# Kernel optimization log

Measured on AMD Instinct MI355X. Metric: run time of the kernel, lower is better.

The kernel has to match this reference:

```python
import jax, jax.numpy as jnp
import numpy as np

N = 20000          # nodes
E = 320000         # edges
G = 256            # g_dim
H1 = 256           # h1_dim (RGCN out)
H2 = 128           # h2_dim (per-head transformer out)
HEADS = 4
R = 8              # num relations
EPS_BN = 1e-5


def setup_inputs() -> dict:
    key = jax.random.key(0)
    ks = jax.random.split(key, 16)
    inp = {
        "node_features": jax.random.normal(ks[0], (N, G), jnp.float32),
        "node_type": jax.random.randint(ks[1], (N,), 0, 3),
        "edge_index": jax.random.randint(ks[2], (2, E), 0, N),
        "edge_type": jax.random.randint(ks[3], (E,), 0, R),
        # RGCNConv params
        "W_rel": jax.random.normal(ks[4], (R, G, H1), jnp.float32) * (1.0 / np.sqrt(G)),
        "W_root": jax.random.normal(ks[5], (G, H1), jnp.float32) * (1.0 / np.sqrt(G)),
        "b_rgcn": jnp.zeros((H1,), jnp.float32),
        # TransformerConv params (concat=True -> HEADS*H2 output)
        "W_q": jax.random.normal(ks[6], (H1, HEADS * H2), jnp.float32) * (1.0 / np.sqrt(H1)),
        "b_q": jnp.zeros((HEADS * H2,), jnp.float32),
        "W_k": jax.random.normal(ks[7], (H1, HEADS * H2), jnp.float32) * (1.0 / np.sqrt(H1)),
        "b_k": jnp.zeros((HEADS * H2,), jnp.float32),
        "W_v": jax.random.normal(ks[8], (H1, HEADS * H2), jnp.float32) * (1.0 / np.sqrt(H1)),
        "b_v": jnp.zeros((HEADS * H2,), jnp.float32),
        "W_skip": jax.random.normal(ks[9], (H1, HEADS * H2), jnp.float32) * (1.0 / np.sqrt(H1)),
        "b_skip": jnp.zeros((HEADS * H2,), jnp.float32),
        # BatchNorm1d params (training-mode batch stats)
        "bn_gamma": jnp.ones((HEADS * H2,), jnp.float32),
        "bn_beta": jnp.zeros((HEADS * H2,), jnp.float32),
    }
    return inp


def reference(node_features, node_type, edge_index, edge_type,
              W_rel, W_root, b_rgcn,
              W_q, b_q, W_k, b_k, W_v, b_v, W_skip, b_skip,
              bn_gamma, bn_beta):
    x = node_features
    src, dst = edge_index[0], edge_index[1]  # messages flow src -> dst

    # ---- RGCNConv (mean aggregation per relation, root weight, bias) ----
    xr = jnp.einsum('nd,rdh->nrh', x, W_rel)           # (N, R, H1)
    msg = xr[src, edge_type]                            # (E, H1)
    seg = dst * R + edge_type                           # combined (node, relation) segment id
    sums = jax.ops.segment_sum(msg, seg, num_segments=N * R)
    cnt = jax.ops.segment_sum(jnp.ones((E,), x.dtype), seg, num_segments=N * R)
    mean = sums / jnp.maximum(cnt, 1.0)[:, None]
    agg = mean.reshape(N, R, H1).sum(axis=1)            # sum over relations
    h1 = agg + x @ W_root + b_rgcn                      # (N, H1)

    # ---- TransformerConv (heads=HEADS, concat=True, root skip) ----
    q = (h1 @ W_q + b_q).reshape(N, HEADS, H2)
    k = (h1 @ W_k + b_k).reshape(N, HEADS, H2)
    v = (h1 @ W_v + b_v).reshape(N, HEADS, H2)

    scale = 1.0 / np.sqrt(H2)
    alpha = jnp.sum(q[dst] * k[src], axis=-1) * scale   # (E, HEADS)
    amax = jax.ops.segment_max(alpha, dst, num_segments=N)  # per-dst softmax max
    ea = jnp.exp(alpha - amax[dst])
    denom = jax.ops.segment_sum(ea, dst, num_segments=N)
    attn = ea / jnp.maximum(denom[dst], 1e-16)          # (E, HEADS)

    out = jax.ops.segment_sum(attn[:, :, None] * v[src], dst, num_segments=N)
    out = out.reshape(N, HEADS * H2) + h1 @ W_skip + b_skip

    # ---- BatchNorm1d (batch stats) + LeakyReLU(0.01) ----
    mu = out.mean(axis=0)
    var = out.var(axis=0)
    xn = (out - mu) * jax.lax.rsqrt(var + EPS_BN)
    y = bn_gamma * xn + bn_beta
    return jax.nn.leaky_relu(y, negative_slope=0.01)
```

## Files before the change

### kernel.cpp

```cpp
#include <hip/hip_runtime.h>

static const int N_NODES = 20000;
static const int N_EDGES = 320000;
static const int GDIM    = 256;
static const int H1DIM   = 256;
static const int C2DIM   = 512;
static const int NREL    = 8;
static const int NSEG    = N_NODES * NREL;

typedef _Float16 __attribute__((ext_vector_type(8))) half8;
typedef _Float16 __attribute__((ext_vector_type(4))) half4;
typedef __attribute__((ext_vector_type(4))) float f32x4;

__device__ __forceinline__ void gload_lds16(const void* g, void* l) {
  __builtin_amdgcn_global_load_lds(
      (const __attribute__((address_space(1))) unsigned int*)g,
      (__attribute__((address_space(3))) unsigned int*)l, 16, 0, 0);
}

__device__ __forceinline__ void swz_bxy(int& bx, int& by) {
  int nx   = gridDim.x;
  int nwg  = nx * gridDim.y;
  int orig = blockIdx.y * nx + blockIdx.x;
  int xcd  = orig & 7;
  int q    = nwg >> 3, r = nwg & 7;
  int base = xcd < r ? xcd * (q + 1) : r * (q + 1) + (xcd - r) * q;
  int wgid = base + (orig >> 3);
  bx = wgid % nx; by = wgid / nx;
}


template<int OUT_HALF>
__global__ __launch_bounds__(256) void gemm_mfma_k(
    const _Float16* __restrict__ A, const _Float16* __restrict__ Bt,
    const float* __restrict__ bias, void* __restrict__ Cout,
    int M, int N, int K)
{
  __shared__ _Float16 As[128 * 64];
  __shared__ _Float16 Bs[128 * 64];
  int bx, by; swz_bxy(bx, by);
  const int tid  = threadIdx.x;
  const int wid  = tid >> 6, lane = tid & 63;
  const int wr   = wid >> 1, wc = wid & 1;
  const int brow = by * 128;
  const int bcol = bx * 128;
  const int l15  = lane & 15, lhi = lane >> 4;
  const int srow = wid * 32;
  const int lrow = lane >> 3;
  const int lchk = lane & 7;

  f32x4 acc[4][4] = {};

  for (int k0 = 0; k0 < K; k0 += 64) {
    __syncthreads();
#pragma unroll
    for (int i = 0; i < 4; ++i) {
      int row = srow + i * 8 + lrow;
      int gc  = lchk ^ (row & 7);
      gload_lds16(A  + (size_t)(brow + row) * K + k0 + gc * 8,
                  &As[(srow + i * 8) * 64]);
      gload_lds16(Bt + (size_t)(bcol + row) * K + k0 + gc * 8,
                  &Bs[(srow + i * 8) * 64]);
    }
    __syncthreads();
#pragma unroll
    for (int kf = 0; kf < 2; ++kf) {
      int cc = kf * 4 + lhi;
      half8 af[4], bfr[4];
#pragma unroll
      for (int mi = 0; mi < 4; ++mi) {
        int row = wr * 64 + mi * 16 + l15;
        af[mi] = ((const half8*)As)[row * 8 + (cc ^ (row & 7))];
      }
#pragma unroll
      for (int ni = 0; ni < 4; ++ni) {
        int row = wc * 64 + ni * 16 + l15;
        bfr[ni] = ((const half8*)Bs)[row * 8 + (cc ^ (row & 7))];
      }
#pragma unroll
      for (int mi = 0; mi < 4; ++mi)
#pragma unroll
        for (int ni = 0; ni < 4; ++ni)
          acc[mi][ni] = __builtin_amdgcn_mfma_f32_16x16x32_f16(
              af[mi], bfr[ni], acc[mi][ni], 0, 0, 0);
    }
  }
#pragma unroll
  for (int ni = 0; ni < 4; ++ni) {
    int col = bcol + wc * 64 + ni * 16 + l15;
    float bb = bias ? bias[col] : 0.f;
#pragma unroll
    for (int mi = 0; mi < 4; ++mi) {
      int row0 = brow + wr * 64 + mi * 16 + lhi * 4;
#pragma unroll
      for (int j = 0; j < 4; ++j) {
        int r = row0 + j;
        if (r >= M) continue;
        float val = acc[mi][ni][j] + bb;
        if (OUT_HALF) ((_Float16*)Cout)[(size_t)r * N + col] = (_Float16)val;
        else          ((float*)Cout)[(size_t)r * N + col] = val;
      }
    }
  }
}

__global__ __launch_bounds__(256) void gemm_qkvs_k(
    const _Float16* __restrict__ A, const _Float16* __restrict__ Bt,
    const float* __restrict__ bias_cat,
    float* __restrict__ qbuf, _Float16* __restrict__ kbuf,
    _Float16* __restrict__ vbuf, float* __restrict__ outp, int M)
{
  const int K = 256, N = 2048;
  __shared__ _Float16 As[128 * 64];
  __shared__ _Float16 Bs[128 * 64];
  int bx, by; swz_bxy(bx, by);
  const int tid  = threadIdx.x;
  const int wid  = tid >> 6, lane = tid & 63;
  const int wr   = wid >> 1, wc = wid & 1;
  const int brow = by * 128;
  const int bcol = bx * 128;
  const int l15  = lane & 15, lhi = lane >> 4;
  const int srow = wid * 32;
  const int lrow = lane >> 3;
  const int lchk = lane & 7;

  f32x4 acc[4][4] = {};

  for (int k0 = 0; k0 < K; k0 += 64) {
    __syncthreads();
#pragma unroll
    for (int i = 0; i < 4; ++i) {
      int row = srow + i * 8 + lrow;
      int gc  = lchk ^ (row & 7);
      gload_lds16(A  + (size_t)(brow + row) * K + k0 + gc * 8,
                  &As[(srow + i * 8) * 64]);
      gload_lds16(Bt + (size_t)(bcol + row) * K + k0 + gc * 8,
                  &Bs[(srow + i * 8) * 64]);
    }
    __syncthreads();
#pragma unroll
    for (int kf = 0; kf < 2; ++kf) {
      int cc = kf * 4 + lhi;
      half8 af[4], bfr[4];
#pragma unroll
      for (int mi = 0; mi < 4; ++mi) {
        int row = wr * 64 + mi * 16 + l15;
        af[mi] = ((const half8*)As)[row * 8 + (cc ^ (row & 7))];
      }
#pragma unroll
      for (int ni = 0; ni < 4; ++ni) {
        int row = wc * 64 + ni * 16 + l15;
        bfr[ni] = ((const half8*)Bs)[row * 8 + (cc ^ (row & 7))];
      }
#pragma unroll
      for (int mi = 0; mi < 4; ++mi)
#pragma unroll
        for (int ni = 0; ni < 4; ++ni)
          acc[mi][ni] = __builtin_amdgcn_mfma_f32_16x16x32_f16(
              af[mi], bfr[ni], acc[mi][ni], 0, 0, 0);
    }
  }
#pragma unroll
  for (int ni = 0; ni < 4; ++ni) {
    int colbase = bcol + wc * 64 + ni * 16;
    int sel = colbase >> 9;
    int c   = (colbase & 511) + l15;
    float bb = bias_cat[colbase + l15];
#pragma unroll
    for (int mi = 0; mi < 4; ++mi) {
      int row0 = brow + wr * 64 + mi * 16 + lhi * 4;
#pragma unroll
      for (int j = 0; j < 4; ++j) {
        int r = row0 + j;
        if (r >= M) continue;
        float val = acc[mi][ni][j] + bb;
        if      (sel == 0) qbuf[(size_t)r * 512 + c] = val;
        else if (sel == 1) kbuf[(size_t)r * 512 + c] = (_Float16)val;
        else if (sel == 2) vbuf[(size_t)r * 512 + c] = (_Float16)val;
        else               outp[(size_t)r * 512 + c] = val;
      }
    }
  }
}

__global__ void conv_wcat_k(const float* __restrict__ W_root, const float* __restrict__ W_rel,
                            _Float16* __restrict__ Wt)
{
  int k = blockIdx.x * 256 + threadIdx.x;
  int n = blockIdx.y;
  float v = (k < 256) ? W_root[(size_t)k * H1DIM + n]
                      : W_rel[(size_t)(k - 256) * H1DIM + n];
  Wt[(size_t)n * 2304 + k] = (_Float16)v;
}

__global__ void conv_wqkvs_k(const float* __restrict__ Wq, const float* __restrict__ Wk,
                             const float* __restrict__ Wv, const float* __restrict__ Ws,
                             const float* __restrict__ bq, const float* __restrict__ bk,
                             const float* __restrict__ bv, const float* __restrict__ bs,
                             _Float16* __restrict__ Wt, float* __restrict__ bias_cat)
{
  int k = threadIdx.x;
  int n = blockIdx.y;
  int sel = n >> 9, c = n & 511;
  const float* W = sel == 0 ? Wq : sel == 1 ? Wk : sel == 2 ? Wv : Ws;
  Wt[(size_t)n * 256 + k] = (_Float16)W[(size_t)k * C2DIM + c];
  if (k == 0) {
    const float* B = sel == 0 ? bq : sel == 1 ? bk : sel == 2 ? bv : bs;
    bias_cat[n] = B[c];
  }
}

__global__ void conv_xh_k(const float* __restrict__ x, _Float16* __restrict__ xh)
{
  int i = blockIdx.x * blockDim.x + threadIdx.x;
  if (i >= N_NODES * GDIM / 4) return;
  float4 v = ((const float4*)x)[i];
  half4 o = {(_Float16)v.x, (_Float16)v.y, (_Float16)v.z, (_Float16)v.w};
  ((half4*)xh)[i] = o;
}

__global__ void hist_k(const int* __restrict__ dst, const int* __restrict__ et,
                       int* __restrict__ h)
{
  int e = blockIdx.x * blockDim.x + threadIdx.x;
  if (e >= N_EDGES) return;
  atomicAdd(&h[dst[e] * NREL + et[e]], 1);
}

__global__ __launch_bounds__(1024) void scan_local_k(
    const int* __restrict__ in, int* __restrict__ out, int* __restrict__ bsum, int n)
{
  __shared__ int s[1024];
  int gi = blockIdx.x * 1024 + threadIdx.x;
  int v = gi < n ? in[gi] : 0;
  s[threadIdx.x] = v; __syncthreads();
  for (int off = 1; off < 1024; off <<= 1) {
    int t = threadIdx.x >= off ? s[threadIdx.x - off] : 0;
    __syncthreads();
    s[threadIdx.x] += t;
    __syncthreads();
  }
  if (gi < n) out[gi] = s[threadIdx.x] - v;
  if (threadIdx.x == 1023) bsum[blockIdx.x] = s[1023];
}

__global__ __launch_bounds__(1024) void scan_small_k(int* __restrict__ bsum, int nb)
{
  __shared__ int s[1024];
  int v = threadIdx.x < nb ? bsum[threadIdx.x] : 0;
  s[threadIdx.x] = v; __syncthreads();
  for (int off = 1; off < 1024; off <<= 1) {
    int t = threadIdx.x >= off ? s[threadIdx.x - off] : 0;
    __syncthreads();
    s[threadIdx.x] += t;
    __syncthreads();
  }
  if (threadIdx.x < nb) bsum[threadIdx.x] = s[threadIdx.x] - v;
}

__global__ void scan_addoff_k(int* __restrict__ out, const int* __restrict__ bsum, int n)
{
  int gi = blockIdx.x * 1024 + threadIdx.x;
  if (gi < n) out[gi] += bsum[blockIdx.x];
}

__global__ void initcur_k(int* __restrict__ off, int* __restrict__ cur)
{
  int i = blockIdx.x * blockDim.x + threadIdx.x;
  if (i < NSEG) cur[i] = off[i];
  if (i == 0) off[NSEG] = N_EDGES;
}

__global__ void reorder_k(const int* __restrict__ src, const int* __restrict__ dst,
                          const int* __restrict__ et,
                          int* __restrict__ cur, int* __restrict__ esrc)
{
  int e = blockIdx.x * blockDim.x + threadIdx.x;
  if (e >= N_EDGES) return;
  int s = src[e];
  int seg = dst[e] * NREL + et[e];
  esrc[atomicAdd(&cur[seg], 1)] = s;
}

__global__ __launch_bounds__(256) void agg_xcat_k(
    const _Float16* __restrict__ xh, const int* __restrict__ off,
    const int* __restrict__ esrc, _Float16* __restrict__ Xcat)
{
  int d = blockIdx.x * 4 + (threadIdx.x >> 6);
  if (d >= N_NODES) return;
  int lane = threadIdx.x & 63;
  _Float16* xrow = Xcat + (size_t)d * 2304;
  half4 xv = ((const half4*)(xh + (size_t)d * GDIM))[lane];
  *(half4*)(xrow + lane * 4) = xv;
  for (int r = 0; r < NREL; ++r) {
    int seg = d * NREL + r;
    int beg = off[seg], end = off[seg + 1];
    float4 acc = make_float4(0.f, 0.f, 0.f, 0.f);
    for (int e = beg; e < end; ++e) {
      int s = esrc[e];
      half4 v = ((const half4*)(xh + (size_t)s * GDIM))[lane];
      acc.x += (float)v.x; acc.y += (float)v.y;
      acc.z += (float)v.z; acc.w += (float)v.w;
    }
    float inv = (end > beg) ? 1.0f / (float)(end - beg) : 0.0f;
    half4 o;
    o.x = (_Float16)(acc.x * inv); o.y = (_Float16)(acc.y * inv);
    o.z = (_Float16)(acc.z * inv); o.w = (_Float16)(acc.w * inv);
    *(half4*)(xrow + 256 + r * 256 + lane * 4) = o;
  }
}

__global__ __launch_bounds__(256) void attn_fused_k(
    const float* __restrict__ q, const _Float16* __restrict__ kb,
    const _Float16* __restrict__ vb,
    const int* __restrict__ off, const int* __restrict__ esrc,
    float* __restrict__ out)
{
  int d = blockIdx.x * 4 + (threadIdx.x >> 6);
  if (d >= N_NODES) return;
  int lane = threadIdx.x & 63;
  const float4* qrow = (const float4*)(q + (size_t)d * C2DIM);
  float4 q0 = qrow[lane * 2], q1 = qrow[lane * 2 + 1];
  float qf[8] = {q0.x, q0.y, q0.z, q0.w, q1.x, q1.y, q1.z, q1.w};
  float m = -3.4e38f, ssum = 0.f;
  float av[8] = {};
  int beg = off[d * NREL], end = off[d * NREL + NREL];
  half8 krN = {}, vrN = {};
  if (beg < end) {
    int s0 = esrc[beg];
    krN = ((const half8*)(kb + (size_t)s0 * C2DIM))[lane];
    vrN = ((const half8*)(vb + (size_t)s0 * C2DIM))[lane];
  }
  for (int e = beg; e < end; ++e) {
    half8 kr = krN, vr = vrN;
    if (e + 1 < end) {
      int s1 = esrc[e + 1];
      krN = ((const half8*)(kb + (size_t)s1 * C2DIM))[lane];
      vrN = ((const half8*)(vb + (size_t)s1 * C2DIM))[lane];
    }
    float p = 0.f;
#pragma unroll
    for (int j = 0; j < 8; ++j) p += qf[j] * (float)kr[j];
    p += __shfl_xor(p, 1); p += __shfl_xor(p, 2);
    p += __shfl_xor(p, 4); p += __shfl_xor(p, 8);
    float a = p * 0.08838834764831845f;
    float mn = fmaxf(m, a);
    float corr = __expf(m - mn), w = __expf(a - mn);
    ssum = ssum * corr + w;
#pragma unroll
    for (int j = 0; j < 8; ++j) av[j] = av[j] * corr + w * (float)vr[j];
    m = mn;
  }
  float inv = 1.0f / fmaxf(ssum, 1e-16f);
  float* orow = out + (size_t)d * C2DIM + lane * 8;
#pragma unroll
  for (int j = 0; j < 8; ++j) orow[j] += av[j] * inv;
}

__global__ __launch_bounds__(512) void bn_stats_k(
    const float* __restrict__ x, float* __restrict__ sums, float* __restrict__ sumsq)
{
  int c = threadIdx.x;
  float s = 0.f, sq = 0.f;
  for (int row = blockIdx.x; row < N_NODES; row += gridDim.x) {
    float v = x[(size_t)row * C2DIM + c];
    s += v; sq += v * v;
  }
  atomicAdd(&sums[c], s);
  atomicAdd(&sumsq[c], sq);
}

__global__ void bn_final_k(const float* __restrict__ sums, const float* __restrict__ sumsq,
                           const float* __restrict__ gamma, const float* __restrict__ beta,
                           float* __restrict__ scale, float* __restrict__ shift)
{
  int c = threadIdx.x;
  float mu  = sums[c] * (1.0f / N_NODES);
  float var = sumsq[c] * (1.0f / N_NODES) - mu * mu;
  float sc  = gamma[c] * rsqrtf(var + 1e-5f);
  scale[c] = sc;
  shift[c] = beta[c] - mu * sc;
}

__global__ void bn_apply_k(float* __restrict__ x, const float* __restrict__ scale,
                           const float* __restrict__ shift, int total)
{
  int i = blockIdx.x * blockDim.x + threadIdx.x;
  if (i >= total) return;
  int c = i & (C2DIM - 1);
  float v = x[i] * scale[c] + shift[c];
  x[i] = v >= 0.f ? v : 0.01f * v;
}

extern "C" void kernel_launch(void* const* d_in, const int* in_sizes, int n_in,
                              void* d_out, int out_size, void* d_ws, size_t ws_size,
                              hipStream_t stream)
{
  const float* x      = (const float*)d_in[0];
  const int*   ei     = (const int*)d_in[2];
  const int*   src    = ei;
  const int*   dst    = ei + N_EDGES;
  const int*   etype  = (const int*)d_in[3];
  const float* W_rel  = (const float*)d_in[4];
  const float* W_root = (const float*)d_in[5];
  const float* b_rgcn = (const float*)d_in[6];
  const float* W_q = (const float*)d_in[7];  const float* b_q = (const float*)d_in[8];
  const float* W_k = (const float*)d_in[9];  const float* b_k = (const float*)d_in[10];
  const float* W_v = (const float*)d_in[11]; const float* b_v = (const float*)d_in[12];
  const float* W_s = (const float*)d_in[13]; const float* b_s = (const float*)d_in[14];
  const float* gamma = (const float*)d_in[15];
  const float* beta  = (const float*)d_in[16];
  float* out = (float*)d_out;

  char* ws = (char*)d_ws;
  _Float16* Xcat   = (_Float16*)(ws + 0);
  float*    qbuf   = (float*)(ws + 0);
  _Float16* kbuf   = (_Float16*)(ws + 40960000);
  _Float16* vbuf   = (_Float16*)(ws + 61440000);
  _Float16* Wt_cat = (_Float16*)(ws + 92160000);
  _Float16* Wt_qk  = (_Float16*)(ws + 93339648);
  _Float16* h1h    = (_Float16*)(ws + 94388224);
  _Float16* xh     = h1h;

  char* C = ws + 104628224;
  int*   cur      = (int*)(C + 0);
  int*   off      = (int*)(C + 640000);
  int*   esrc     = (int*)(C + 1280016);
  int*   bsum     = (int*)(C + 2560016);
  float* bns      = (float*)(C + 2564112);
  float* bias_cat = (float*)(C + 2572304);
  float* bnsum = bns, *bnsq = bns + 512, *bnscale = bns + 1024, *bnshift = bns + 1536;

  hipMemsetAsync(C, 0, 640000, stream);
  hipMemsetAsync(bns, 0, 8192, stream);

  dim3 blk(256);
  const int NB = (NSEG + 1023) / 1024;

  hist_k<<<dim3((N_EDGES + 255) / 256), blk, 0, stream>>>(dst, etype, cur);
  scan_local_k<<<dim3(NB), dim3(1024), 0, stream>>>(cur, off, bsum, NSEG);
  scan_small_k<<<dim3(1), dim3(1024), 0, stream>>>(bsum, NB);
  scan_addoff_k<<<dim3(NB), dim3(1024), 0, stream>>>(off, bsum, NSEG);
  initcur_k<<<dim3((NSEG + 255) / 256), blk, 0, stream>>>(off, cur);
  reorder_k<<<dim3((N_EDGES + 255) / 256), blk, 0, stream>>>(
      src, dst, etype, cur, esrc);

  conv_wcat_k<<<dim3(9, 256), blk, 0, stream>>>(W_root, W_rel, Wt_cat);
  conv_wqkvs_k<<<dim3(1, 2048), blk, 0, stream>>>(
      W_q, W_k, W_v, W_s, b_q, b_k, b_v, b_s, Wt_qk, bias_cat);
  conv_xh_k<<<dim3((N_NODES * GDIM / 4 + 255) / 256), blk, 0, stream>>>(x, xh);

  agg_xcat_k<<<dim3((N_NODES + 3) / 4), blk, 0, stream>>>(xh, off, esrc, Xcat);

  gemm_mfma_k<1><<<dim3(H1DIM / 128, (N_NODES + 127) / 128), blk, 0, stream>>>(
      Xcat, Wt_cat, b_rgcn, h1h, N_NODES, H1DIM, 2304);

  gemm_qkvs_k<<<dim3(2048 / 128, (N_NODES + 127) / 128), blk, 0, stream>>>(
      h1h, Wt_qk, bias_cat, qbuf, kbuf, vbuf, out, N_NODES);

  attn_fused_k<<<dim3((N_NODES + 3) / 4), blk, 0, stream>>>(
      qbuf, kbuf, vbuf, off, esrc, out);

  bn_stats_k<<<dim3(208), dim3(512), 0, stream>>>(out, bnsum, bnsq);
  bn_final_k<<<dim3(1), dim3(512), 0, stream>>>(bnsum, bnsq, gamma, beta, bnscale, bnshift);
  bn_apply_k<<<dim3((N_NODES * C2DIM + 255) / 256), blk, 0, stream>>>(
      out, bnscale, bnshift, N_NODES * C2DIM);
}
```

Measured before the change: 391.4 us.

## Merge prep kernels, store QKVS interleaved in fp16, fuse BN finalize and skip add

Merges the histogram, the weight transposes and the x-to-half conversion into one prep kernel, and folds initcur into scan_addoff. The QKVS GEMM now writes one interleaved fp16 row per node through the generic GEMM. Attention reads q, k, v and skip from that buffer and writes the output directly instead of read-modify-write. BatchNorm finalize moves into a vectorized apply kernel. Together these remove several launches and a memset and cut memory traffic, at the cost of fp16 precision for q and the skip path.

```diff
diff --git a/kernel.cpp b/kernel.cpp
--- a/kernel.cpp
+++ b/kernel.cpp
@@ -28,7 +28,6 @@
   int wgid = base + (orig >> 3);
   bx = wgid % nx; by = wgid / nx;
 }
-
 
 template<int OUT_HALF>
 __global__ __launch_bounds__(256) void gemm_mfma_k(
@@ -104,127 +103,43 @@
   }
 }
 
-__global__ __launch_bounds__(256) void gemm_qkvs_k(
-    const _Float16* __restrict__ A, const _Float16* __restrict__ Bt,
-    const float* __restrict__ bias_cat,
-    float* __restrict__ qbuf, _Float16* __restrict__ kbuf,
-    _Float16* __restrict__ vbuf, float* __restrict__ outp, int M)
-{
-  const int K = 256, N = 2048;
-  __shared__ _Float16 As[128 * 64];
-  __shared__ _Float16 Bs[128 * 64];
-  int bx, by; swz_bxy(bx, by);
-  const int tid  = threadIdx.x;
-  const int wid  = tid >> 6, lane = tid & 63;
-  const int wr   = wid >> 1, wc = wid & 1;
-  const int brow = by * 128;
-  const int bcol = bx * 128;
-  const int l15  = lane & 15, lhi = lane >> 4;
-  const int srow = wid * 32;
-  const int lrow = lane >> 3;
-  const int lchk = lane & 7;
-
-  f32x4 acc[4][4] = {};
-
-  for (int k0 = 0; k0 < K; k0 += 64) {
-    __syncthreads();
-#pragma unroll
-    for (int i = 0; i < 4; ++i) {
-      int row = srow + i * 8 + lrow;
-      int gc  = lchk ^ (row & 7);
-      gload_lds16(A  + (size_t)(brow + row) * K + k0 + gc * 8,
-                  &As[(srow + i * 8) * 64]);
-      gload_lds16(Bt + (size_t)(bcol + row) * K + k0 + gc * 8,
-                  &Bs[(srow + i * 8) * 64]);
-    }
-    __syncthreads();
-#pragma unroll
-    for (int kf = 0; kf < 2; ++kf) {
-      int cc = kf * 4 + lhi;
-      half8 af[4], bfr[4];
-#pragma unroll
-      for (int mi = 0; mi < 4; ++mi) {
-        int row = wr * 64 + mi * 16 + l15;
-        af[mi] = ((const half8*)As)[row * 8 + (cc ^ (row & 7))];
-      }
-#pragma unroll
-      for (int ni = 0; ni < 4; ++ni) {
-        int row = wc * 64 + ni * 16 + l15;
-        bfr[ni] = ((const half8*)Bs)[row * 8 + (cc ^ (row & 7))];
-      }
-#pragma unroll
-      for (int mi = 0; mi < 4; ++mi)
-#pragma unroll
-        for (int ni = 0; ni < 4; ++ni)
-          acc[mi][ni] = __builtin_amdgcn_mfma_f32_16x16x32_f16(
-              af[mi], bfr[ni], acc[mi][ni], 0, 0, 0);
-    }
-  }
-#pragma unroll
-  for (int ni = 0; ni < 4; ++ni) {
-    int colbase = bcol + wc * 64 + ni * 16;
-    int sel = colbase >> 9;
-    int c   = (colbase & 511) + l15;
-    float bb = bias_cat[colbase + l15];
-#pragma unroll
-    for (int mi = 0; mi < 4; ++mi) {
-      int row0 = brow + wr * 64 + mi * 16 + lhi * 4;
-#pragma unroll
-      for (int j = 0; j < 4; ++j) {
-        int r = row0 + j;
-        if (r >= M) continue;
-        float val = acc[mi][ni][j] + bb;
-        if      (sel == 0) qbuf[(size_t)r * 512 + c] = val;
-        else if (sel == 1) kbuf[(size_t)r * 512 + c] = (_Float16)val;
-        else if (sel == 2) vbuf[(size_t)r * 512 + c] = (_Float16)val;
-        else               outp[(size_t)r * 512 + c] = val;
-      }
-    }
-  }
-}
-
-__global__ void conv_wcat_k(const float* __restrict__ W_root, const float* __restrict__ W_rel,
-                            _Float16* __restrict__ Wt)
-{
-  int k = blockIdx.x * 256 + threadIdx.x;
-  int n = blockIdx.y;
-  float v = (k < 256) ? W_root[(size_t)k * H1DIM + n]
-                      : W_rel[(size_t)(k - 256) * H1DIM + n];
-  Wt[(size_t)n * 2304 + k] = (_Float16)v;
-}
-
-__global__ void conv_wqkvs_k(const float* __restrict__ Wq, const float* __restrict__ Wk,
-                             const float* __restrict__ Wv, const float* __restrict__ Ws,
-                             const float* __restrict__ bq, const float* __restrict__ bk,
-                             const float* __restrict__ bv, const float* __restrict__ bs,
-                             _Float16* __restrict__ Wt, float* __restrict__ bias_cat)
-{
-  int k = threadIdx.x;
-  int n = blockIdx.y;
-  int sel = n >> 9, c = n & 511;
-  const float* W = sel == 0 ? Wq : sel == 1 ? Wk : sel == 2 ? Wv : Ws;
-  Wt[(size_t)n * 256 + k] = (_Float16)W[(size_t)k * C2DIM + c];
-  if (k == 0) {
-    const float* B = sel == 0 ? bq : sel == 1 ? bk : sel == 2 ? bv : bs;
-    bias_cat[n] = B[c];
-  }
-}
-
-__global__ void conv_xh_k(const float* __restrict__ x, _Float16* __restrict__ xh)
-{
-  int i = blockIdx.x * blockDim.x + threadIdx.x;
-  if (i >= N_NODES * GDIM / 4) return;
-  float4 v = ((const float4*)x)[i];
-  half4 o = {(_Float16)v.x, (_Float16)v.y, (_Float16)v.z, (_Float16)v.w};
-  ((half4*)xh)[i] = o;
-}
-
-__global__ void hist_k(const int* __restrict__ dst, const int* __restrict__ et,
-                       int* __restrict__ h)
-{
-  int e = blockIdx.x * blockDim.x + threadIdx.x;
-  if (e >= N_EDGES) return;
-  atomicAdd(&h[dst[e] * NREL + et[e]], 1);
+__global__ __launch_bounds__(256) void prep_k(
+    const int* __restrict__ dst, const int* __restrict__ et, int* __restrict__ hist,
+    const float* __restrict__ W_root, const float* __restrict__ W_rel,
+    _Float16* __restrict__ Wt_cat,
+    const float* __restrict__ Wq, const float* __restrict__ Wk,
+    const float* __restrict__ Wv, const float* __restrict__ Ws,
+    const float* __restrict__ bq, const float* __restrict__ bk,
+    const float* __restrict__ bv, const float* __restrict__ bs,
+    _Float16* __restrict__ Wt_qk, float* __restrict__ bias_cat,
+    const float* __restrict__ x, _Float16* __restrict__ xh)
+{
+  int b = blockIdx.x, tid = threadIdx.x;
+  if (b < 1250) {
+    int e = b * 256 + tid;
+    if (e < N_EDGES) atomicAdd(&hist[dst[e] * NREL + et[e]], 1);
+  } else if (b < 3554) {
+    int idx = (b - 1250) * 256 + tid;
+    int k = idx % 2304, n = idx / 2304;
+    float v = (k < 256) ? W_root[(size_t)k * H1DIM + n]
+                        : W_rel[(size_t)(k - 256) * H1DIM + n];
+    Wt_cat[(size_t)n * 2304 + k] = (_Float16)v;
+  } else if (b < 5602) {
+    int idx = (b - 3554) * 256 + tid;
+    int n = idx >> 8, k = idx & 255;
+    int sel = n >> 9, c = n & 511;
+    const float* W = sel == 0 ? Wq : sel == 1 ? Wk : sel == 2 ? Wv : Ws;
+    Wt_qk[(size_t)n * 256 + k] = (_Float16)W[(size_t)k * C2DIM + c];
+    if (k == 0) {
+      const float* B = sel == 0 ? bq : sel == 1 ? bk : sel == 2 ? bv : bs;
+      bias_cat[n] = B[c];
+    }
+  } else {
+    int i = (b - 5602) * 256 + tid;
+    float4 v = ((const float4*)x)[i];
+    half4 o = {(_Float16)v.x, (_Float16)v.y, (_Float16)v.z, (_Float16)v.w};
+    ((half4*)xh)[i] = o;
+  }
 }
 
 __global__ __launch_bounds__(1024) void scan_local_k(
@@ -258,17 +173,16 @@
   if (threadIdx.x < nb) bsum[threadIdx.x] = s[threadIdx.x] - v;
 }
 
-__global__ void scan_addoff_k(int* __restrict__ out, const int* __restrict__ bsum, int n)
+__global__ void scan_addoff_k(int* __restrict__ off, const int* __restrict__ bsum,
+                              int* __restrict__ cur, int n)
 {
   int gi = blockIdx.x * 1024 + threadIdx.x;
-  if (gi < n) out[gi] += bsum[blockIdx.x];
-}
-
-__global__ void initcur_k(int* __restrict__ off, int* __restrict__ cur)
-{
-  int i = blockIdx.x * blockDim.x + threadIdx.x;
-  if (i < NSEG) cur[i] = off[i];
-  if (i == 0) off[NSEG] = N_EDGES;
+  if (gi < n) {
+    int v = off[gi] + bsum[blockIdx.x];
+    off[gi] = v;
+    cur[gi] = v;
+  }
+  if (gi == 0) off[n] = N_EDGES;
 }
 
 __global__ void reorder_k(const int* __restrict__ src, const int* __restrict__ dst,
@@ -277,9 +191,8 @@
 {
   int e = blockIdx.x * blockDim.x + threadIdx.x;
   if (e >= N_EDGES) return;
-  int s = src[e];
   int seg = dst[e] * NREL + et[e];
-  esrc[atomicAdd(&cur[seg], 1)] = s;
+  esrc[atomicAdd(&cur[seg], 1)] = src[e];
 }
 
 __global__ __launch_bounds__(256) void agg_xcat_k(
@@ -311,32 +224,34 @@
 }
 
 __global__ __launch_bounds__(256) void attn_fused_k(
-    const float* __restrict__ q, const _Float16* __restrict__ kb,
-    const _Float16* __restrict__ vb,
+    const _Float16* __restrict__ qkvs,
     const int* __restrict__ off, const int* __restrict__ esrc,
     float* __restrict__ out)
 {
   int d = blockIdx.x * 4 + (threadIdx.x >> 6);
   if (d >= N_NODES) return;
   int lane = threadIdx.x & 63;
-  const float4* qrow = (const float4*)(q + (size_t)d * C2DIM);
-  float4 q0 = qrow[lane * 2], q1 = qrow[lane * 2 + 1];
-  float qf[8] = {q0.x, q0.y, q0.z, q0.w, q1.x, q1.y, q1.z, q1.w};
+  half8 qr = ((const half8*)(qkvs + (size_t)d * 2048))[lane];
+  float qf[8];
+#pragma unroll
+  for (int j = 0; j < 8; ++j) qf[j] = (float)qr[j];
   float m = -3.4e38f, ssum = 0.f;
   float av[8] = {};
   int beg = off[d * NREL], end = off[d * NREL + NREL];
   half8 krN = {}, vrN = {};
   if (beg < end) {
     int s0 = esrc[beg];
-    krN = ((const half8*)(kb + (size_t)s0 * C2DIM))[lane];
-    vrN = ((const half8*)(vb + (size_t)s0 * C2DIM))[lane];
+    const half8* row = (const half8*)(qkvs + (size_t)s0 * 2048 + 512);
+    krN = row[lane];
+    vrN = row[64 + lane];
   }
   for (int e = beg; e < end; ++e) {
     half8 kr = krN, vr = vrN;
     if (e + 1 < end) {
       int s1 = esrc[e + 1];
-      krN = ((const half8*)(kb + (size_t)s1 * C2DIM))[lane];
-      vrN = ((const half8*)(vb + (size_t)s1 * C2DIM))[lane];
+      const half8* row = (const half8*)(qkvs + (size_t)s1 * 2048 + 512);
+      krN = row[lane];
+      vrN = row[64 + lane];
     }
     float p = 0.f;
 #pragma unroll
@@ -352,9 +267,10 @@
     m = mn;
   }
   float inv = 1.0f / fmaxf(ssum, 1e-16f);
+  half8 sr = ((const half8*)(qkvs + (size_t)d * 2048 + 1536))[lane];
   float* orow = out + (size_t)d * C2DIM + lane * 8;
 #pragma unroll
-  for (int j = 0; j < 8; ++j) orow[j] += av[j] * inv;
+  for (int j = 0; j < 8; ++j) orow[j] = av[j] * inv + (float)sr[j];
 }
 
 __global__ __launch_bounds__(512) void bn_stats_k(
@@ -370,26 +286,26 @@
   atomicAdd(&sumsq[c], sq);
 }
 
-__global__ void bn_final_k(const float* __restrict__ sums, const float* __restrict__ sumsq,
+__global__ void bn_apply_k(float* __restrict__ x,
+                           const float* __restrict__ sums, const float* __restrict__ sumsq,
                            const float* __restrict__ gamma, const float* __restrict__ beta,
-                           float* __restrict__ scale, float* __restrict__ shift)
-{
-  int c = threadIdx.x;
-  float mu  = sums[c] * (1.0f / N_NODES);
-  float var = sumsq[c] * (1.0f / N_NODES) - mu * mu;
-  float sc  = gamma[c] * rsqrtf(var + 1e-5f);
-  scale[c] = sc;
-  shift[c] = beta[c] - mu * sc;
-}
-
-__global__ void bn_apply_k(float* __restrict__ x, const float* __restrict__ scale,
-                           const float* __restrict__ shift, int total)
+                           int total4)
 {
   int i = blockIdx.x * blockDim.x + threadIdx.x;
-  if (i >= total) return;
-  int c = i & (C2DIM - 1);
-  float v = x[i] * scale[c] + shift[c];
-  x[i] = v >= 0.f ? v : 0.01f * v;
+  if (i >= total4) return;
+  int c0 = (i & 127) * 4;
+  float4 v = ((const float4*)x)[i];
+  float o[4] = {v.x, v.y, v.z, v.w};
+#pragma unroll
+  for (int j = 0; j < 4; ++j) {
+    int c = c0 + j;
+    float mu  = sums[c] * (1.0f / N_NODES);
+    float var = sumsq[c] * (1.0f / N_NODES) - mu * mu;
+    float sc  = gamma[c] * rsqrtf(var + 1e-5f);
+    float val = (o[j] - mu) * sc + beta[c];
+    o[j] = val >= 0.f ? val : 0.01f * val;
+  }
+  ((float4*)x)[i] = make_float4(o[0], o[1], o[2], o[3]);
 }
 
 extern "C" void kernel_launch(void* const* d_in, const int* in_sizes, int n_in,
@@ -414,9 +330,7 @@
 
   char* ws = (char*)d_ws;
   _Float16* Xcat   = (_Float16*)(ws + 0);
-  float*    qbuf   = (float*)(ws + 0);
-  _Float16* kbuf   = (_Float16*)(ws + 40960000);
-  _Float16* vbuf   = (_Float16*)(ws + 61440000);
+  _Float16* QKVS   = (_Float16*)(ws + 0);
   _Float16* Wt_cat = (_Float16*)(ws + 92160000);
   _Float16* Wt_qk  = (_Float16*)(ws + 93339648);
   _Float16* h1h    = (_Float16*)(ws + 94388224);
@@ -424,45 +338,41 @@
 
   char* C = ws + 104628224;
   int*   cur      = (int*)(C + 0);
-  int*   off      = (int*)(C + 640000);
-  int*   esrc     = (int*)(C + 1280016);
-  int*   bsum     = (int*)(C + 2560016);
-  float* bns      = (float*)(C + 2564112);
-  float* bias_cat = (float*)(C + 2572304);
-  float* bnsum = bns, *bnsq = bns + 512, *bnscale = bns + 1024, *bnshift = bns + 1536;
-
-  hipMemsetAsync(C, 0, 640000, stream);
-  hipMemsetAsync(bns, 0, 8192, stream);
+  float* bns      = (float*)(C + 640000);
+  float* bias_cat = (float*)(C + 648192);
+  int*   off      = (int*)(C + 656384);
+  int*   esrc     = (int*)(C + 1296400);
+  int*   bsum     = (int*)(C + 2576400);
+  float* bnsum = bns, *bnsq = bns + 512;
+
+  hipMemsetAsync(C, 0, 648192, stream);
 
   dim3 blk(256);
   const int NB = (NSEG + 1023) / 1024;
 
-  hist_k<<<dim3((N_EDGES + 255) / 256), blk, 0, stream>>>(dst, etype, cur);
+  prep_k<<<dim3(10602), blk, 0, stream>>>(
+      dst, etype, cur,
+      W_root, W_rel, Wt_cat,
+      W_q, W_k, W_v, W_s, b_q, b_k, b_v, b_s, Wt_qk, bias_cat,
+      x, xh);
+
   scan_local_k<<<dim3(NB), dim3(1024), 0, stream>>>(cur, off, bsum, NSEG);
   scan_small_k<<<dim3(1), dim3(1024), 0, stream>>>(bsum, NB);
-  scan_addoff_k<<<dim3(NB), dim3(1024), 0, stream>>>(off, bsum, NSEG);
-  initcur_k<<<dim3((NSEG + 255) / 256), blk, 0, stream>>>(off, cur);
+  scan_addoff_k<<<dim3(NB), dim3(1024), 0, stream>>>(off, bsum, cur, NSEG);
   reorder_k<<<dim3((N_EDGES + 255) / 256), blk, 0, stream>>>(
       src, dst, etype, cur, esrc);
 
-  conv_wcat_k<<<dim3(9, 256), blk, 0, stream>>>(W_root, W_rel, Wt_cat);
-  conv_wqkvs_k<<<dim3(1, 2048), blk, 0, stream>>>(
-      W_q, W_k, W_v, W_s, b_q, b_k, b_v, b_s, Wt_qk, bias_cat);
-  conv_xh_k<<<dim3((N_NODES * GDIM / 4 + 255) / 256), blk, 0, stream>>>(x, xh);
-
   agg_xcat_k<<<dim3((N_NODES + 3) / 4), blk, 0, stream>>>(xh, off, esrc, Xcat);
 
   gemm_mfma_k<1><<<dim3(H1DIM / 128, (N_NODES + 127) / 128), blk, 0, stream>>>(
       Xcat, Wt_cat, b_rgcn, h1h, N_NODES, H1DIM, 2304);
 
-  gemm_qkvs_k<<<dim3(2048 / 128, (N_NODES + 127) / 128), blk, 0, stream>>>(
-      h1h, Wt_qk, bias_cat, qbuf, kbuf, vbuf, out, N_NODES);
-
-  attn_fused_k<<<dim3((N_NODES + 3) / 4), blk, 0, stream>>>(
-      qbuf, kbuf, vbuf, off, esrc, out);
+  gemm_mfma_k<1><<<dim3(2048 / 128, (N_NODES + 127) / 128), blk, 0, stream>>>(
+      h1h, Wt_qk, bias_cat, QKVS, N_NODES, 2048, 256);
+
+  attn_fused_k<<<dim3((N_NODES + 3) / 4), blk, 0, stream>>>(QKVS, off, esrc, out);
 
   bn_stats_k<<<dim3(208), dim3(512), 0, stream>>>(out, bnsum, bnsq);
-  bn_final_k<<<dim3(1), dim3(512), 0, stream>>>(bnsum, bnsq, gamma, beta, bnscale, bnshift);
-  bn_apply_k<<<dim3((N_NODES * C2DIM + 255) / 256), blk, 0, stream>>>(
-      out, bnscale, bnshift, N_NODES * C2DIM);
-}
+  bn_apply_k<<<dim3((N_NODES * C2DIM / 4 + 255) / 256), blk, 0, stream>>>(
+      out, bnsum, bnsq, gamma, beta, N_NODES * C2DIM / 4);
+}
```

Measured after the change: 357.6 us. -8.6%, faster.
